# Performance work log

Hardware: AMD Instinct MI355X
Metric: run time of the kernel (lower is better)

## Reference

```python
import jax, jax.numpy as jnp
import numpy as np

BS, NS, D, H = 4, 1024, 2048, 16
DH = D // H
SCALE = DH ** -0.5
MASK_BIAS = -1e9


def setup_inputs() -> dict:
    key = jax.random.key(0)
    k1, k2, k3, k4, k5 = jax.random.split(key, 5)
    x = jax.random.normal(k1, (BS, NS, D), dtype=jnp.float32)
    attention_ids = jax.random.randint(k2, (BS, NS), 0, 2, dtype=jnp.int32)
    # torch.nn.Linear weights: [out_features, in_features]
    w_in = jax.random.normal(k3, (3 * D, D), dtype=jnp.float32) * (D ** -0.5)
    w_out = jax.random.normal(k4, (D, D), dtype=jnp.float32) * (D ** -0.5)
    b_out = jax.random.normal(k5, (D,), dtype=jnp.float32) * 0.02
    return {"x": x, "attention_ids": attention_ids, "w_in": w_in,
            "w_out": w_out, "b_out": b_out}


def reference(x, attention_ids, w_in, w_out, b_out):
    bs, ns, _ = x.shape
    qkv = jnp.einsum('bsd,ed->bse', x, w_in)            # [bs, ns, 3*D]
    qkv = qkv.reshape(bs, ns, 3, H, DH).transpose(2, 0, 3, 1, 4)
    q, k, v = qkv[0], qkv[1], qkv[2]                     # [bs, H, ns, DH]
    attn = jnp.einsum('bhqd,bhkd->bhqk', q, k)           # [bs, H, ns, ns]
    # NOTE: mask bias added BEFORE the scale multiply, as in the source.
    bias = (attention_ids.astype(attn.dtype) * MASK_BIAS)[:, None, None, :]
    attn = jax.nn.softmax((attn + bias) * SCALE, axis=-1)
    out = jnp.einsum('bhqk,bhkd->bhqd', attn, v)         # [bs, H, ns, DH]
    out = out.transpose(0, 2, 1, 3).reshape(bs, ns, D)
    return jnp.einsum('bsd,ed->bse', out, w_out) + b_out
```

## Files before the change

kernel.cpp:

```cpp
#include <hip/hip_runtime.h>
#include <hip/hip_bf16.h>
#include <stdint.h>

typedef __bf16 bf16;
typedef __bf16 bf16x8 __attribute__((ext_vector_type(8)));
typedef __bf16 bf16x4 __attribute__((ext_vector_type(4)));
typedef float floatx4 __attribute__((ext_vector_type(4)));

#define NSEQ   1024
#define DM     2048
#define NH     16
#define DHD    128
#define E3     6144
#define SCALE_F 0.08838834764831845f
#define MBIAS_S (-1.0e9f * SCALE_F)
#define NEG_HUGE (-3.0e38f)
#define DEFER_THR 8.0f

static __device__ __forceinline__ floatx4 mfma16(bf16x8 a, bf16x8 b, floatx4 c) {
  return __builtin_amdgcn_mfma_f32_16x16x32_bf16(a, b, c, 0, 0, 0);
}

static __device__ __forceinline__ void load_lds16(const bf16* g, bf16* l) {
  __builtin_amdgcn_global_load_lds(
      (__attribute__((address_space(1))) const void*)g,
      (__attribute__((address_space(3))) void*)l, 16, 0, 0);
}

#define SCHED0 __builtin_amdgcn_sched_barrier(0)

__global__ __launch_bounds__(256) void cast3_kernel(
    const float* __restrict__ x, const float* __restrict__ wi,
    const float* __restrict__ wo, bf16* __restrict__ xb,
    bf16* __restrict__ wib, bf16* __restrict__ wob) {
  const int blk = blockIdx.x;
  const float* src;
  bf16* dst;
  int base;
  if (blk < 8192)       { src = x;  dst = xb;  base = blk; }
  else if (blk < 20480) { src = wi; dst = wib; base = blk - 8192; }
  else                  { src = wo; dst = wob; base = blk - 20480; }
  const int i = base * 256 + threadIdx.x;
  float4 v = ((const float4*)src)[i];
  bf16x4 o;
  o[0] = (bf16)v.x; o[1] = (bf16)v.y; o[2] = (bf16)v.z; o[3] = (bf16)v.w;
  ((bf16x4*)dst)[i] = o;
}

template <typename OutT>
__global__ __launch_bounds__(512) void gemm256_bt_kernel(
    const bf16* __restrict__ A, const bf16* __restrict__ B,
    OutT* __restrict__ C, const float* __restrict__ bias,
    int N, int K, bf16* __restrict__ vt) {
  __shared__ __align__(16) bf16 Al[2][2][256 * 32];
  __shared__ __align__(16) bf16 Bl[2][2][256 * 32];
  const int NT = K >> 6;
  const int ntn = N >> 8;
  const int tm = blockIdx.x / ntn;
  const int tn = blockIdx.x - tm * ntn;
  const int tid = threadIdx.x;
  const int w = tid >> 6, lane = tid & 63;
  const int lq = lane & 15, lg = lane >> 4;
  const int wr = w >> 2, wc = w & 3;
  const int sub = lane >> 2;
  const int cpl = (lane & 3) ^ ((lane >> 3) & 3);
  const int scp8 = (lg ^ ((lq >> 1) & 3)) << 3;

  const bf16* Ag = A + (size_t)(tm * 256) * K;
  const bf16* Bg = B + (size_t)(tn * 256) * K;

  auto STAGE = [&](const bf16* G, bf16* Ldst, int kcol) {
#pragma unroll
    for (int j = 0; j < 2; j++) {
      const int r0 = w * 32 + j * 16;
      load_lds16(G + (size_t)(r0 + sub) * K + kcol + cpl * 8, Ldst + r0 * 32);
    }
  };
  auto RD = [&](const bf16* slot, int rbase) -> bf16x8 {
    return *(const bf16x8*)(slot + (rbase + lq) * 32 + scp8);
  };

  floatx4 acc[8][4] = {};

  STAGE(Ag, Al[0][0], 0);
  STAGE(Bg, Bl[0][0], 0);
  STAGE(Ag, Al[0][1], 32);
  STAGE(Bg, Bl[0][1], 32);
  STAGE(Ag, Al[1][0], 64);
  STAGE(Bg, Bl[1][0], 64);
  asm volatile("s_waitcnt vmcnt(8)" ::: "memory");
  SCHED0;
  __builtin_amdgcn_s_barrier();
  SCHED0;

  int buf = 0;
  for (int kt = 0; kt < NT; ++kt) {
    const int nb = buf ^ 1;
    const int k1 = ((kt + 1 < NT) ? kt + 1 : NT - 1) << 6;
    const int k2 = ((kt + 2 < NT) ? kt + 2 : NT - 1) << 6;
    bf16x8 af[8], bfr[4];

#pragma unroll
    for (int ni = 0; ni < 4; ni++) bfr[ni] = RD(Bl[buf][0], wc * 64 + ni * 16);
#pragma unroll
    for (int mi = 0; mi < 8; mi++) af[mi] = RD(Al[buf][0], wr * 128 + mi * 16);
    STAGE(Ag, Al[nb][1], k1 + 32);
    STAGE(Bg, Bl[nb][1], k1 + 32);
    SCHED0; __builtin_amdgcn_s_barrier(); SCHED0;
    __builtin_amdgcn_s_setprio(1);
#pragma unroll
    for (int mi = 0; mi < 8; mi++)
#pragma unroll
      for (int ni = 0; ni < 4; ni++)
        acc[mi][ni] = mfma16(af[mi], bfr[ni], acc[mi][ni]);
    __builtin_amdgcn_s_setprio(0);
    asm volatile("s_waitcnt vmcnt(8)" ::: "memory");
    SCHED0; __builtin_amdgcn_s_barrier(); SCHED0;

#pragma unroll
    for (int ni = 0; ni < 4; ni++) bfr[ni] = RD(Bl[buf][1], wc * 64 + ni * 16);
#pragma unroll
    for (int mi = 0; mi < 8; mi++) af[mi] = RD(Al[buf][1], wr * 128 + mi * 16);
    STAGE(Ag, Al[buf][0], k2);
    STAGE(Bg, Bl[buf][0], k2);
    SCHED0; __builtin_amdgcn_s_barrier(); SCHED0;
    __builtin_amdgcn_s_setprio(1);
#pragma unroll
    for (int mi = 0; mi < 8; mi++)
#pragma unroll
      for (int ni = 0; ni < 4; ni++)
        acc[mi][ni] = mfma16(af[mi], bfr[ni], acc[mi][ni]);
    __builtin_amdgcn_s_setprio(0);
    asm volatile("s_waitcnt vmcnt(8)" ::: "memory");
    SCHED0; __builtin_amdgcn_s_barrier(); SCHED0;

    buf = nb;
  }
  asm volatile("s_waitcnt vmcnt(0)" ::: "memory");

  if (vt != nullptr && tn >= 16) {
    const int b = tm >> 2;
    const int sb = (tm & 3) * 256 + wr * 128 + lg * 4;
    const int head2 = (tn - 16) * 2;
#pragma unroll
    for (int ni = 0; ni < 4; ni++) {
      const int col = wc * 64 + ni * 16 + lq;
      bf16* vdst = vt + ((size_t)(b * NH + head2 + (col >> 7)) * DHD +
                         (col & 127)) * NSEQ + sb;
#pragma unroll
      for (int m = 0; m < 8; m++) {
        bf16x4 o;
#pragma unroll
        for (int r = 0; r < 4; r++) o[r] = (bf16)acc[m][ni][r];
        *(bf16x4*)(vdst + m * 16) = o;
      }
    }
  } else {
#pragma unroll
    for (int ni = 0; ni < 4; ni++) {
      const int col = tn * 256 + wc * 64 + ni * 16 + lq;
      const float bv = bias ? bias[col] : 0.f;
#pragma unroll
      for (int m = 0; m < 8; m++) {
        const size_t rb = (size_t)(tm * 256 + wr * 128 + m * 16 + lg * 4);
#pragma unroll
        for (int r = 0; r < 4; r++)
          C[(rb + r) * N + col] = (OutT)(acc[m][ni][r] + bv);
      }
    }
  }
}

template <typename OutT>
__global__ __launch_bounds__(256) void gemm_bt_kernel(
    const bf16* __restrict__ A, const bf16* __restrict__ B,
    OutT* __restrict__ C, const float* __restrict__ bias,
    int N, int K) {
  __shared__ bf16 As[128 * 32];
  __shared__ bf16 Bs[128 * 32];
  const int ntn = N >> 7;
  const int tm = blockIdx.x / ntn;
  const int tn = blockIdx.x - tm * ntn;
  const int tid = threadIdx.x;
  const int w = tid >> 6;
  const int lane = tid & 63;
  const int lq = lane & 15;
  const int lg = lane >> 4;
  const int wr = w >> 1;
  const int wc = w & 1;

  const bf16* Ag = A + (size_t)(tm * 128) * K;
  const bf16* Bg = B + (size_t)(tn * 128) * K;
  const int c0 = tid, c1 = tid + 256;
  const int r0 = c0 >> 2, o0 = (c0 & 3) * 8;
  const int r1 = c1 >> 2, o1 = (c1 & 3) * 8;
  bf16* lA0 = As + w * 512;
  bf16* lA1 = As + w * 512 + 2048;
  bf16* lB0 = Bs + w * 512;
  bf16* lB1 = Bs + w * 512 + 2048;

  floatx4 acc[4][4] = {};

  for (int k0 = 0; k0 < K; k0 += 32) {
    load_lds16(Ag + (size_t)r0 * K + k0 + o0, lA0);
    load_lds16(Ag + (size_t)r1 * K + k0 + o1, lA1);
    load_lds16(Bg + (size_t)r0 * K + k0 + o0, lB0);
    load_lds16(Bg + (size_t)r1 * K + k0 + o1, lB1);
    __syncthreads();
    bf16x8 af[4], bfr[4];
#pragma unroll
    for (int m = 0; m < 4; m++)
      af[m] = *(const bf16x8*)(As + (wr * 64 + m * 16 + lq) * 32 + lg * 8);
#pragma unroll
    for (int n = 0; n < 4; n++)
      bfr[n] = *(const bf16x8*)(Bs + (wc * 64 + n * 16 + lq) * 32 + lg * 8);
#pragma unroll
    for (int m = 0; m < 4; m++)
#pragma unroll
      for (int n = 0; n < 4; n++)
        acc[m][n] = mfma16(af[m], bfr[n], acc[m][n]);
    __syncthreads();
  }

#pragma unroll
  for (int n = 0; n < 4; n++) {
    const int ccol = tn * 128 + wc * 64 + n * 16 + lq;
    const float bv = bias ? bias[ccol] : 0.f;
#pragma unroll
    for (int m = 0; m < 4; m++) {
      const size_t rbase = (size_t)(tm * 128 + wr * 64 + m * 16 + lg * 4);
#pragma unroll
      for (int r = 0; r < 4; r++)
        C[(rbase + r) * N + ccol] = (OutT)(acc[m][n][r] + bv);
    }
  }
}

__global__ __launch_bounds__(256) void attn_kernel(
    const bf16* __restrict__ qkv, const bf16* __restrict__ vt,
    const int* __restrict__ ids, bf16* __restrict__ ao) {
  __shared__ bf16 Ksh[2][64 * 128];
  __shared__ bf16 Vsh[2][128 * 64];
  __shared__ bf16 plds[4][16][72];
  const int bid = (blockIdx.x & 7) * 128 + (blockIdx.x >> 3);
  const int qt = bid & 15;
  const int h = (bid >> 4) & 15;
  const int b = bid >> 8;
  const int tid = threadIdx.x;
  const int w = tid >> 6;
  const int lane = tid & 63;
  const int lq = lane & 15;
  const int lg = lane >> 4;
  const int q0 = qt * 64 + w * 16;
  const int swz = (lq & 7) << 4;

  const int krow0 = w * 16 + (lane >> 4);
  const int kc = lane & 15;
  const int vrow0 = w * 32 + (lane >> 3);
  const int vc = lane & 7;
  const int vr7 = (lane >> 3) & 7;

  const bf16* kg = qkv + DM + h * DHD;
  const bf16* vg = vt + (size_t)(b * NH + h) * DHD * NSEQ;

  auto stage = [&](int buf, int k0) {
#pragma unroll
    for (int i = 0; i < 4; i++) {
      const int kr = krow0 + i * 4;
      load_lds16(kg + (size_t)(b * NSEQ + k0 + kr) * E3 + ((kc ^ (kr & 7)) * 8),
                 &Ksh[buf][(w * 16 + i * 4) * 128]);
    }
#pragma unroll
    for (int i = 0; i < 4; i++) {
      const int vr = vrow0 + i * 8;
      load_lds16(vg + (size_t)vr * NSEQ + k0 + ((vc ^ vr7) * 8),
                 &Vsh[buf][(w * 32 + i * 8) * 64]);
    }
  };

  bf16x8 qf[4];
  const bf16* qb = qkv + (size_t)(b * NSEQ + q0 + lq) * E3 + h * DHD + lg * 8;
#pragma unroll
  for (int kk = 0; kk < 4; kk++) qf[kk] = *(const bf16x8*)(qb + kk * 32);

  floatx4 acc[8] = {};
  float M[4], L[4];
#pragma unroll
  for (int r = 0; r < 4; r++) { M[r] = NEG_HUGE; L[r] = 0.f; }

  bf16 (*pw)[72] = plds[w];
  const int* idb = ids + b * NSEQ;

  stage(0, 0);
  __syncthreads();
  int cur = 0;

  for (int t = 0; t < 16; t++) {
    const int k0 = t * 64;
    if (t < 15) stage(cur ^ 1, k0 + 64);

    const bf16* Kc = Ksh[cur];
    floatx4 s[4] = {};
    __builtin_amdgcn_s_setprio(1);
#pragma unroll
    for (int n = 0; n < 4; n++) {
      const int krow = n * 16 + lq;
#pragma unroll
      for (int kk = 0; kk < 4; kk++) {
        bf16x8 kf = *(const bf16x8*)(Kc + krow * 128 +
                                     (((kk * 64 + lg * 16) ^ swz) >> 1));
        s[n] = mfma16(qf[kk], kf, s[n]);
      }
    }
    __builtin_amdgcn_s_setprio(0);
    float sa[4][4], pm[4];
#pragma unroll
    for (int r = 0; r < 4; r++) pm[r] = NEG_HUGE;
#pragma unroll
    for (int n = 0; n < 4; n++) {
      const float bv = idb[k0 + n * 16 + lq] ? MBIAS_S : 0.f;
#pragma unroll
      for (int r = 0; r < 4; r++) {
        sa[n][r] = s[n][r] * SCALE_F + bv;
        pm[r] = fmaxf(pm[r], sa[n][r]);
      }
    }
#pragma unroll
    for (int m = 1; m <= 8; m <<= 1)
#pragma unroll
      for (int r = 0; r < 4; r++) pm[r] = fmaxf(pm[r], __shfl_xor(pm[r], m, 64));

    int grew = 0;
#pragma unroll
    for (int r = 0; r < 4; r++) grew |= (pm[r] > M[r] + DEFER_THR) ? 1 : 0;
    const bool full = __any(grew);
    float corr[4];
    if (full) {
#pragma unroll
      for (int r = 0; r < 4; r++) {
        const float mn = fmaxf(M[r], pm[r]);
        corr[r] = __expf(M[r] - mn);
        M[r] = mn;
      }
    }
    float rs[4] = {0.f, 0.f, 0.f, 0.f};
#pragma unroll
    for (int n = 0; n < 4; n++)
#pragma unroll
      for (int r = 0; r < 4; r++) {
        const float p = __expf(sa[n][r] - M[r]);
        sa[n][r] = p;
        rs[r] += p;
      }
#pragma unroll
    for (int m = 1; m <= 8; m <<= 1)
#pragma unroll
      for (int r = 0; r < 4; r++) rs[r] += __shfl_xor(rs[r], m, 64);
    if (full) {
#pragma unroll
      for (int r = 0; r < 4; r++) L[r] = L[r] * corr[r] + rs[r];
#pragma unroll
      for (int n8 = 0; n8 < 8; n8++)
#pragma unroll
        for (int r = 0; r < 4; r++) acc[n8][r] *= corr[r];
    } else {
#pragma unroll
      for (int r = 0; r < 4; r++) L[r] += rs[r];
    }
#pragma unroll
    for (int n = 0; n < 4; n++)
#pragma unroll
      for (int r = 0; r < 4; r++) pw[lg * 4 + r][n * 16 + lq] = (bf16)sa[n][r];
    bf16x8 pf0 = *(const bf16x8*)(&pw[lq][lg * 8]);
    bf16x8 pf1 = *(const bf16x8*)(&pw[lq][32 + lg * 8]);
    const bf16* Vc = Vsh[cur];
    __builtin_amdgcn_s_setprio(1);
#pragma unroll
    for (int n8 = 0; n8 < 8; n8++) {
      const int vrow = n8 * 16 + lq;
      bf16x8 v0 = *(const bf16x8*)(Vc + vrow * 64 + (((lg * 16) ^ swz) >> 1));
      bf16x8 v1 = *(const bf16x8*)(Vc + vrow * 64 + (((64 + lg * 16) ^ swz) >> 1));
      acc[n8] = mfma16(pf0, v0, acc[n8]);
      acc[n8] = mfma16(pf1, v1, acc[n8]);
    }
    __builtin_amdgcn_s_setprio(0);
    __syncthreads();
    cur ^= 1;
  }

  float inv[4];
#pragma unroll
  for (int r = 0; r < 4; r++) inv[r] = 1.f / L[r];
  bf16* aob = ao + (size_t)(b * NSEQ + q0 + lg * 4) * DM + h * DHD + lq;
#pragma unroll
  for (int n8 = 0; n8 < 8; n8++)
#pragma unroll
    for (int r = 0; r < 4; r++)
      aob[(size_t)r * DM + n8 * 16] = (bf16)(acc[n8][r] * inv[r]);
}

extern "C" void kernel_launch(void* const* d_in, const int* in_sizes, int n_in,
                              void* d_out, int out_size, void* d_ws, size_t ws_size,
                              hipStream_t stream) {
  const float* x     = (const float*)d_in[0];
  const int*   ids   = (const int*)d_in[1];
  const float* w_in  = (const float*)d_in[2];
  const float* w_out = (const float*)d_in[3];
  const float* b_out = (const float*)d_in[4];
  float* out = (float*)d_out;

  bf16* ws  = (bf16*)d_ws;
  bf16* xb  = ws;
  bf16* wib = xb  + (size_t)4096 * 2048;
  bf16* wob = wib + (size_t)6144 * 2048;
  bf16* qkv = wob + (size_t)2048 * 2048;
  bf16* vtb = qkv + (size_t)4096 * 6144;
  bf16* aob = vtb + (size_t)4 * 16 * 128 * 1024;

  cast3_kernel<<<24576, 256, 0, stream>>>(x, w_in, w_out, xb, wib, wob);
  gemm256_bt_kernel<bf16><<<16 * 24, 512, 0, stream>>>(xb, wib, qkv, nullptr,
                                                       6144, 2048, vtb);
  attn_kernel<<<1024, 256, 0, stream>>>(qkv, vtb, ids, aob);
  gemm_bt_kernel<float><<<32 * 16, 256, 0, stream>>>(aob, wob, out, b_out, 2048, 2048);
}
```

Baseline: 292.4 us.

## Process two query tiles per attention block to reuse staged K/V

Result: slower. 317.7 us (+8.6%).

```diff
diff --git a/kernel.cpp b/kernel.cpp
--- a/kernel.cpp
+++ b/kernel.cpp
@@ -242,16 +242,15 @@
   __shared__ bf16 Ksh[2][64 * 128];
   __shared__ bf16 Vsh[2][128 * 64];
   __shared__ bf16 plds[4][16][72];
-  const int bid = (blockIdx.x & 7) * 128 + (blockIdx.x >> 3);
-  const int qt = bid & 15;
-  const int h = (bid >> 4) & 15;
-  const int b = bid >> 8;
+  const int bid = (blockIdx.x & 7) * 64 + (blockIdx.x >> 3);
+  const int qp = bid & 7;
+  const int h = (bid >> 3) & 15;
+  const int b = bid >> 7;
   const int tid = threadIdx.x;
   const int w = tid >> 6;
   const int lane = tid & 63;
   const int lq = lane & 15;
   const int lg = lane >> 4;
-  const int q0 = qt * 64 + w * 16;
   const int swz = (lq & 7) << 4;
 
   const int krow0 = w * 16 + (lane >> 4);
@@ -278,15 +277,21 @@
     }
   };
 
-  bf16x8 qf[4];
-  const bf16* qb = qkv + (size_t)(b * NSEQ + q0 + lq) * E3 + h * DHD + lg * 8;
-#pragma unroll
-  for (int kk = 0; kk < 4; kk++) qf[kk] = *(const bf16x8*)(qb + kk * 32);
-
-  floatx4 acc[8] = {};
-  float M[4], L[4];
-#pragma unroll
-  for (int r = 0; r < 4; r++) { M[r] = NEG_HUGE; L[r] = 0.f; }
+  bf16x8 qf[2][4];
+#pragma unroll
+  for (int g = 0; g < 2; g++) {
+    const int q0 = (qp + g * 8) * 64 + w * 16;
+    const bf16* qb = qkv + (size_t)(b * NSEQ + q0 + lq) * E3 + h * DHD + lg * 8;
+#pragma unroll
+    for (int kk = 0; kk < 4; kk++) qf[g][kk] = *(const bf16x8*)(qb + kk * 32);
+  }
+
+  floatx4 acc[2][8] = {};
+  float M[2][4], L[2][4];
+#pragma unroll
+  for (int g = 0; g < 2; g++)
+#pragma unroll
+    for (int r = 0; r < 4; r++) { M[g][r] = NEG_HUGE; L[g][r] = 0.f; }
 
   bf16 (*pw)[72] = plds[w];
   const int* idb = ids + b * NSEQ;
@@ -300,103 +305,114 @@
     if (t < 15) stage(cur ^ 1, k0 + 64);
 
     const bf16* Kc = Ksh[cur];
-    floatx4 s[4] = {};
-    __builtin_amdgcn_s_setprio(1);
-#pragma unroll
-    for (int n = 0; n < 4; n++) {
-      const int krow = n * 16 + lq;
-#pragma unroll
-      for (int kk = 0; kk < 4; kk++) {
-        bf16x8 kf = *(const bf16x8*)(Kc + krow * 128 +
-                                     (((kk * 64 + lg * 16) ^ swz) >> 1));
-        s[n] = mfma16(qf[kk], kf, s[n]);
-      }
-    }
-    __builtin_amdgcn_s_setprio(0);
-    float sa[4][4], pm[4];
-#pragma unroll
-    for (int r = 0; r < 4; r++) pm[r] = NEG_HUGE;
-#pragma unroll
-    for (int n = 0; n < 4; n++) {
-      const float bv = idb[k0 + n * 16 + lq] ? MBIAS_S : 0.f;
-#pragma unroll
-      for (int r = 0; r < 4; r++) {
-        sa[n][r] = s[n][r] * SCALE_F + bv;
-        pm[r] = fmaxf(pm[r], sa[n][r]);
-      }
-    }
-#pragma unroll
-    for (int m = 1; m <= 8; m <<= 1)
-#pragma unroll
-      for (int r = 0; r < 4; r++) pm[r] = fmaxf(pm[r], __shfl_xor(pm[r], m, 64));
-
-    int grew = 0;
-#pragma unroll
-    for (int r = 0; r < 4; r++) grew |= (pm[r] > M[r] + DEFER_THR) ? 1 : 0;
-    const bool full = __any(grew);
-    float corr[4];
-    if (full) {
-#pragma unroll
-      for (int r = 0; r < 4; r++) {
-        const float mn = fmaxf(M[r], pm[r]);
-        corr[r] = __expf(M[r] - mn);
-        M[r] = mn;
-      }
-    }
-    float rs[4] = {0.f, 0.f, 0.f, 0.f};
-#pragma unroll
-    for (int n = 0; n < 4; n++)
-#pragma unroll
-      for (int r = 0; r < 4; r++) {
-        const float p = __expf(sa[n][r] - M[r]);
-        sa[n][r] = p;
-        rs[r] += p;
-      }
-#pragma unroll
-    for (int m = 1; m <= 8; m <<= 1)
-#pragma unroll
-      for (int r = 0; r < 4; r++) rs[r] += __shfl_xor(rs[r], m, 64);
-    if (full) {
-#pragma unroll
-      for (int r = 0; r < 4; r++) L[r] = L[r] * corr[r] + rs[r];
-#pragma unroll
-      for (int n8 = 0; n8 < 8; n8++)
-#pragma unroll
-        for (int r = 0; r < 4; r++) acc[n8][r] *= corr[r];
-    } else {
-#pragma unroll
-      for (int r = 0; r < 4; r++) L[r] += rs[r];
-    }
-#pragma unroll
-    for (int n = 0; n < 4; n++)
-#pragma unroll
-      for (int r = 0; r < 4; r++) pw[lg * 4 + r][n * 16 + lq] = (bf16)sa[n][r];
-    bf16x8 pf0 = *(const bf16x8*)(&pw[lq][lg * 8]);
-    bf16x8 pf1 = *(const bf16x8*)(&pw[lq][32 + lg * 8]);
     const bf16* Vc = Vsh[cur];
-    __builtin_amdgcn_s_setprio(1);
-#pragma unroll
-    for (int n8 = 0; n8 < 8; n8++) {
-      const int vrow = n8 * 16 + lq;
-      bf16x8 v0 = *(const bf16x8*)(Vc + vrow * 64 + (((lg * 16) ^ swz) >> 1));
-      bf16x8 v1 = *(const bf16x8*)(Vc + vrow * 64 + (((64 + lg * 16) ^ swz) >> 1));
-      acc[n8] = mfma16(pf0, v0, acc[n8]);
-      acc[n8] = mfma16(pf1, v1, acc[n8]);
-    }
-    __builtin_amdgcn_s_setprio(0);
+#pragma unroll
+    for (int g = 0; g < 2; g++) {
+      floatx4 s[4] = {};
+      __builtin_amdgcn_s_setprio(1);
+#pragma unroll
+      for (int n = 0; n < 4; n++) {
+        const int krow = n * 16 + lq;
+#pragma unroll
+        for (int kk = 0; kk < 4; kk++) {
+          bf16x8 kf = *(const bf16x8*)(Kc + krow * 128 +
+                                       (((kk * 64 + lg * 16) ^ swz) >> 1));
+          s[n] = mfma16(qf[g][kk], kf, s[n]);
+        }
+      }
+      __builtin_amdgcn_s_setprio(0);
+      float sa[4][4], pm[4];
+#pragma unroll
+      for (int r = 0; r < 4; r++) pm[r] = NEG_HUGE;
+#pragma unroll
+      for (int n = 0; n < 4; n++) {
+        const float bv = idb[k0 + n * 16 + lq] ? MBIAS_S : 0.f;
+#pragma unroll
+        for (int r = 0; r < 4; r++) {
+          sa[n][r] = s[n][r] * SCALE_F + bv;
+          pm[r] = fmaxf(pm[r], sa[n][r]);
+        }
+      }
+#pragma unroll
+      for (int m = 1; m <= 8; m <<= 1)
+#pragma unroll
+        for (int r = 0; r < 4; r++)
+          pm[r] = fmaxf(pm[r], __shfl_xor(pm[r], m, 64));
+
+      int grew = 0;
+#pragma unroll
+      for (int r = 0; r < 4; r++)
+        grew |= (pm[r] > M[g][r] + DEFER_THR) ? 1 : 0;
+      const bool full = __any(grew);
+      float corr[4];
+      if (full) {
+#pragma unroll
+        for (int r = 0; r < 4; r++) {
+          const float mn = fmaxf(M[g][r], pm[r]);
+          corr[r] = __expf(M[g][r] - mn);
+          M[g][r] = mn;
+        }
+      }
+      float rs[4] = {0.f, 0.f, 0.f, 0.f};
+#pragma unroll
+      for (int n = 0; n < 4; n++)
+#pragma unroll
+        for (int r = 0; r < 4; r++) {
+          const float p = __expf(sa[n][r] - M[g][r]);
+          sa[n][r] = p;
+          rs[r] += p;
+        }
+#pragma unroll
+      for (int m = 1; m <= 8; m <<= 1)
+#pragma unroll
+        for (int r = 0; r < 4; r++) rs[r] += __shfl_xor(rs[r], m, 64);
+      if (full) {
+#pragma unroll
+        for (int r = 0; r < 4; r++) L[g][r] = L[g][r] * corr[r] + rs[r];
+#pragma unroll
+        for (int n8 = 0; n8 < 8; n8++)
+#pragma unroll
+          for (int r = 0; r < 4; r++) acc[g][n8][r] *= corr[r];
+      } else {
+#pragma unroll
+        for (int r = 0; r < 4; r++) L[g][r] += rs[r];
+      }
+#pragma unroll
+      for (int n = 0; n < 4; n++)
+#pragma unroll
+        for (int r = 0; r < 4; r++)
+          pw[lg * 4 + r][n * 16 + lq] = (bf16)sa[n][r];
+      bf16x8 pf0 = *(const bf16x8*)(&pw[lq][lg * 8]);
+      bf16x8 pf1 = *(const bf16x8*)(&pw[lq][32 + lg * 8]);
+      __builtin_amdgcn_s_setprio(1);
+#pragma unroll
+      for (int n8 = 0; n8 < 8; n8++) {
+        const int vrow = n8 * 16 + lq;
+        bf16x8 v0 = *(const bf16x8*)(Vc + vrow * 64 + (((lg * 16) ^ swz) >> 1));
+        bf16x8 v1 = *(const bf16x8*)(Vc + vrow * 64 +
+                                     (((64 + lg * 16) ^ swz) >> 1));
+        acc[g][n8] = mfma16(pf0, v0, acc[g][n8]);
+        acc[g][n8] = mfma16(pf1, v1, acc[g][n8]);
+      }
+      __builtin_amdgcn_s_setprio(0);
+    }
     __syncthreads();
     cur ^= 1;
   }
 
-  float inv[4];
-#pragma unroll
-  for (int r = 0; r < 4; r++) inv[r] = 1.f / L[r];
-  bf16* aob = ao + (size_t)(b * NSEQ + q0 + lg * 4) * DM + h * DHD + lq;
-#pragma unroll
-  for (int n8 = 0; n8 < 8; n8++)
-#pragma unroll
-    for (int r = 0; r < 4; r++)
-      aob[(size_t)r * DM + n8 * 16] = (bf16)(acc[n8][r] * inv[r]);
+#pragma unroll
+  for (int g = 0; g < 2; g++) {
+    float inv[4];
+#pragma unroll
+    for (int r = 0; r < 4; r++) inv[r] = 1.f / L[g][r];
+    const int q0 = (qp + g * 8) * 64 + w * 16;
+    bf16* aob = ao + (size_t)(b * NSEQ + q0 + lg * 4) * DM + h * DHD + lq;
+#pragma unroll
+    for (int n8 = 0; n8 < 8; n8++)
+#pragma unroll
+      for (int r = 0; r < 4; r++)
+        aob[(size_t)r * DM + n8 * 16] = (bf16)(acc[g][n8][r] * inv[r]);
+  }
 }
 
 extern "C" void kernel_launch(void* const* d_in, const int* in_sizes, int n_in,
@@ -420,6 +436,6 @@
   cast3_kernel<<<24576, 256, 0, stream>>>(x, w_in, w_out, xb, wib, wob);
   gemm256_bt_kernel<bf16><<<16 * 24, 512, 0, stream>>>(xb, wib, qkv, nullptr,
                                                        6144, 2048, vtb);
-  attn_kernel<<<1024, 256, 0, stream>>>(qkv, vtb, ids, aob);
+  attn_kernel<<<512, 256, 0, stream>>>(qkv, vtb, ids, aob);
   gemm_bt_kernel<float><<<32 * 16, 256, 0, stream>>>(aob, wob, out, b_out, 2048, 2048);
 }
```
